# Kernel tuning notes

Measured on AMD Instinct MI355X. Metric: run time of the kernel, lower is better.

The kernel has to match this reference:

```python
import jax, jax.numpy as jnp
import numpy as np

B, T, D = 16, 512, 512
MEL_MAX = 4096


def setup_inputs() -> dict:
    key = jax.random.key(0)
    k0, k1, k2, k3 = jax.random.split(key, 4)
    x = jax.random.normal(k0, (B, T, D), dtype=jnp.float32)
    # integer frame durations per phoneme (the `target` used in training-mode LR)
    target = jax.random.randint(k1, (B, T), 0, 8, dtype=jnp.int32)
    scale = 1.0 / np.sqrt(D)
    W1 = jax.random.normal(k2, (D, D), dtype=jnp.float32) * scale
    b1 = jnp.zeros((D,), dtype=jnp.float32)
    W2 = jax.random.normal(k3, (D, 1), dtype=jnp.float32) * scale
    b2 = jnp.zeros((1,), dtype=jnp.float32)
    return {"x": x, "W1": W1, "b1": b1, "W2": W2, "b2": b2,
            "target": target, "mel_max_length": MEL_MAX}


def _length_regulate(x, durations, mel_max_length):
    """Vectorized repeat_interleave + pad.
    x: [B,T,D] float, durations: [B,T] int, output: [B,mel_max_length,D].
    Equivalent to per-batch torch expand+cat then pad, done via cumsum+searchsorted gather.
    """
    cs = jnp.cumsum(durations, axis=1)                    # [B,T] exclusive upper bounds
    pos = jnp.arange(mel_max_length)                      # [L]

    def expand_one(xb, csb):
        idx = jnp.searchsorted(csb, pos, side='right')    # [L] phoneme index per frame
        valid = pos < csb[-1]                             # frames beyond total -> pad
        idx = jnp.clip(idx, 0, xb.shape[0] - 1)
        return jnp.where(valid[:, None], xb[idx], jnp.zeros((), xb.dtype))

    return jax.vmap(expand_one)(x, cs)                    # [B,L,D]


def reference(x, W1, b1, W2, b2, target, mel_max_length):
    # DurationPredictor: Linear(512,512)+ReLU, Linear(512,1)+ReLU, squeeze -> [B,T]
    h = jax.nn.relu(jnp.einsum('btd,de->bte', x, W1) + b1)
    duration_predictor_output = jax.nn.relu(jnp.einsum('bte,eo->bto', h, W2) + b2)[..., 0]
    # Training-mode LR: expand x by integer `target` durations, pad to mel_max_length
    output = _length_regulate(x, target, mel_max_length)
    return output, duration_predictor_output
```

## Files before the change

### kernel.cpp

```cpp
#include <hip/hip_runtime.h>
#include <hip/hip_bf16.h>

#define BSZ 16
#define TT 512
#define DD 512
#define MM (BSZ * TT)
#define NPART 8
#define NMEGA 512

typedef __attribute__((ext_vector_type(8))) short bf16x8;
typedef __attribute__((ext_vector_type(8))) unsigned short ushort8;
typedef __attribute__((ext_vector_type(4))) float f32x4;

__global__ __launch_bounds__(256) void prep_kernel(const float* __restrict__ W1,
                                                   const int* __restrict__ target,
                                                   ushort* __restrict__ wth,
                                                   int* __restrict__ imap, int L) {
    int bid = blockIdx.x;
    if (bid < 256) {
        int t = bid * 256 + threadIdx.x;
        int n  = t & (DD - 1);
        int kq = t >> 9;
        ushort hh[4];
        #pragma unroll
        for (int i = 0; i < 4; ++i) {
            float f = W1[(size_t)(kq * 4 + i) * DD + n];
            __hip_bfloat16 bh = __float2bfloat16(f);
            hh[i] = *(ushort*)&bh;
        }
        ((ushort4*)wth)[(size_t)n * (DD / 4) + kq] = make_ushort4(hh[0], hh[1], hh[2], hh[3]);
    } else {
        int b = bid - 256;
        __shared__ int s[TT];
        int t = threadIdx.x;
        s[t]       = target[b * TT + t];
        s[t + 256] = target[b * TT + t + 256];
        __syncthreads();
        #pragma unroll
        for (int off = 1; off < TT; off <<= 1) {
            int v0 = (t >= off) ? s[t - off] : 0;
            int v1 = s[t + 256 - off];
            __syncthreads();
            s[t] += v0;
            s[t + 256] += v1;
            __syncthreads();
        }
        int total = s[TT - 1];
        int* imb = imap + (size_t)b * L;
        for (int ph = t; ph < TT; ph += 256) {
            int st = (ph == 0) ? 0 : s[ph - 1];
            int en = s[ph];
            for (int d = st; d < en; ++d) imb[d] = ph;
        }
        for (int l = total + t; l < L; l += 256) imb[l] = -1;
    }
}

#define BM 64
#define BN 128
#define BK 64
__global__ __launch_bounds__(256, 2) void mega_kernel(const ushort* __restrict__ wth,
                                                      const float* __restrict__ b1,
                                                      const float* __restrict__ W2,
                                                      const float* __restrict__ x,
                                                      const int* __restrict__ imap,
                                                      float* __restrict__ out,
                                                      float* __restrict__ partial,
                                                      int L) {
    __shared__ ushort ldsA[2][BM * 64];
    __shared__ ushort ldsB[2][BN * 64];
    const int bid = blockIdx.x;
    const int t = threadIdx.x;
    const int lane = t & 63, wave = t >> 6;
    const int row0 = (bid >> 2) * BM;
    const int col0 = (bid & 3) * BN;
    const int rq = t >> 3;
    const int ls = (t & 7) ^ (rq & 7);
    const int sco = ls * 8;
    const int ar = t >> 2;
    const int ac = (t & 3) * 16;

    const int b_lr    = bid >> 5;
    const int chunk0  = (bid & 31) * 128;
    const int lr_lane = t & 127;
    const int lr_half = t >> 7;
    const f32x4* x4g = (const f32x4*)(x + (size_t)b_lr * TT * DD);
    f32x4*       o4  = (f32x4*)(out + (size_t)b_lr * L * DD);
    const int*   imb = imap + (size_t)b_lr * L;

    auto stageB = [&](int buf, int kt) {
        const int k0 = kt * BK;
        #pragma unroll
        for (int q = 0; q < 4; ++q) {
            int row = q * 32 + rq;
            const ushort* gb = wth + (size_t)(col0 + row) * DD + k0 + sco;
            auto lb = (__attribute__((address_space(3))) unsigned int*)
                      ((char*)&ldsB[buf][0] + q * 4096 + wave * 1024);
            __builtin_amdgcn_global_load_lds(
                (const __attribute__((address_space(1))) unsigned int*)gb, lb, 16, 0, 0);
        }
    };
    auto stageA = [&](int buf, int kt) {
        const float* xa = x + (size_t)(row0 + ar) * DD + kt * BK + ac;
        float fl[16];
        *(f32x4*)&fl[0]  = ((const f32x4*)xa)[0];
        *(f32x4*)&fl[4]  = ((const f32x4*)xa)[1];
        *(f32x4*)&fl[8]  = ((const f32x4*)xa)[2];
        *(f32x4*)&fl[12] = ((const f32x4*)xa)[3];
        ushort us[16];
        #pragma unroll
        for (int j = 0; j < 16; ++j) {
            __hip_bfloat16 bh = __float2bfloat16(fl[j]);
            us[j] = *(ushort*)&bh;
        }
        int s0 = ((t & 3) * 2)     ^ (ar & 7);
        int s1 = ((t & 3) * 2 + 1) ^ (ar & 7);
        *(ushort8*)&ldsA[buf][ar * 64 + s0 * 8] = *(ushort8*)&us[0];
        *(ushort8*)&ldsA[buf][ar * 64 + s1 * 8] = *(ushort8*)&us[8];
    };

    const int wm = (wave >> 1) * 32;
    const int wn = (wave & 1) * 64;
    const int l15 = lane & 15, l4 = lane >> 4;
    f32x4 acc[2][4] = {};

    stageB(0, 0);
    stageA(0, 0);
    __syncthreads();
    int cur = 0;
    #pragma unroll 1
    for (int kt = 0; kt < DD / BK; ++kt) {
        if (kt + 1 < DD / BK) stageB(cur ^ 1, kt + 1);

        const int rb0 = chunk0 + kt * 16 + lr_half;
        int idxs[8];
        #pragma unroll
        for (int p = 0; p < 8; ++p) idxs[p] = imb[rb0 + p * 2];
        f32x4 gv[8];
        #pragma unroll
        for (int p = 0; p < 8; ++p)
            gv[p] = (idxs[p] >= 0) ? x4g[(size_t)idxs[p] * (DD / 4) + lr_lane]
                                   : (f32x4){0.f, 0.f, 0.f, 0.f};

        const ushort* At = &ldsA[cur][0];
        const ushort* Bt = &ldsB[cur][0];
        bf16x8 a[2][2], b[4][2];
        #pragma unroll
        for (int i = 0; i < 2; ++i) {
            int r = wm + i * 16 + l15;
            #pragma unroll
            for (int ks = 0; ks < 2; ++ks) {
                int sl = (ks * 4 + l4) ^ (r & 7);
                a[i][ks] = *(const bf16x8*)&At[r * 64 + sl * 8];
            }
        }
        #pragma unroll
        for (int j = 0; j < 4; ++j) {
            int r = wn + j * 16 + l15;
            #pragma unroll
            for (int ks = 0; ks < 2; ++ks) {
                int sl = (ks * 4 + l4) ^ (r & 7);
                b[j][ks] = *(const bf16x8*)&Bt[r * 64 + sl * 8];
            }
        }
        #pragma unroll
        for (int ks = 0; ks < 2; ++ks)
            #pragma unroll
            for (int i = 0; i < 2; ++i)
                #pragma unroll
                for (int j = 0; j < 4; ++j)
                    acc[i][j] = __builtin_amdgcn_mfma_f32_16x16x32_bf16(a[i][ks], b[j][ks], acc[i][j], 0, 0, 0);

        if (kt + 1 < DD / BK) stageA(cur ^ 1, kt + 1);

        #pragma unroll
        for (int p = 0; p < 8; ++p)
            __builtin_nontemporal_store(gv[p], &o4[(size_t)(rb0 + p * 2) * (DD / 4) + lr_lane]);

        __syncthreads();
        cur ^= 1;
    }

    const int pslice = (bid & 3) * 2 + (wn >> 6);
    #pragma unroll
    for (int i = 0; i < 2; ++i) {
        #pragma unroll
        for (int r = 0; r < 4; ++r) {
            float s = 0.f;
            #pragma unroll
            for (int j = 0; j < 4; ++j) {
                int cg = col0 + wn + j * 16 + l15;
                float h = acc[i][j][r] + b1[cg];
                h = fmaxf(h, 0.f);
                s += h * W2[cg];
            }
            s += __shfl_xor(s, 1);
            s += __shfl_xor(s, 2);
            s += __shfl_xor(s, 4);
            s += __shfl_xor(s, 8);
            if (l15 == 0) {
                int rg = row0 + wm + i * 16 + l4 * 4 + r;
                partial[(size_t)pslice * MM + rg] = s;
            }
        }
    }
}

__global__ __launch_bounds__(256) void dpo_kernel(const float* __restrict__ partial,
                                                  const float* __restrict__ b2,
                                                  float* __restrict__ dpo) {
    int m = blockIdx.x * 256 + threadIdx.x;
    float s = b2[0];
    #pragma unroll
    for (int nb = 0; nb < NPART; ++nb) s += partial[(size_t)nb * MM + m];
    dpo[m] = fmaxf(s, 0.f);
}

extern "C" void kernel_launch(void* const* d_in, const int* in_sizes, int n_in,
                              void* d_out, int out_size, void* d_ws, size_t ws_size,
                              hipStream_t stream) {
    const float* x      = (const float*)d_in[0];
    const float* W1     = (const float*)d_in[1];
    const float* b1     = (const float*)d_in[2];
    const float* W2     = (const float*)d_in[3];
    const float* b2     = (const float*)d_in[4];
    const int*   target = (const int*)d_in[5];
    int L = (out_size - BSZ * TT) / (BSZ * DD);

    float* out_lr  = (float*)d_out;
    float* out_dpo = (float*)d_out + (size_t)BSZ * L * DD;

    ushort* wth     = (ushort*)d_ws;
    float*  partial = (float*)(wth + (size_t)DD * DD);
    int*    imap    = (int*)(partial + (size_t)NPART * MM);

    prep_kernel<<<dim3(272), dim3(256), 0, stream>>>(W1, target, wth, imap, L);
    mega_kernel<<<dim3(NMEGA), dim3(256), 0, stream>>>(wth, b1, W2, x, imap,
                                                       out_lr, partial, L);
    dpo_kernel<<<dim3(MM / 256), dim3(256), 0, stream>>>(partial, b2, out_dpo);
}
```

Baseline: 43.04 us.

## Split mega kernel into independent GEMM waves and gather waves without LDS

Restructures the fused kernel so each block's first two waves each compute an independent 32x64 GEMM tile, reading A and B fragments straight from global memory with no LDS staging or barriers. The other two waves handle the length-regulation gather/copy on their own row chunks. The grid doubles to 1024 blocks and launch bounds allow 4 blocks per CU. This removes the __syncthreads coupling between the GEMM and the memory-bound copy, but drops LDS reuse, so operand reads come redundantly from global or L2.

```diff
diff --git a/kernel.cpp b/kernel.cpp
--- a/kernel.cpp
+++ b/kernel.cpp
@@ -6,10 +6,9 @@
 #define DD 512
 #define MM (BSZ * TT)
 #define NPART 8
-#define NMEGA 512
+#define NMEGA 1024
 
 typedef __attribute__((ext_vector_type(8))) short bf16x8;
-typedef __attribute__((ext_vector_type(8))) unsigned short ushort8;
 typedef __attribute__((ext_vector_type(4))) float f32x4;
 
 __global__ __launch_bounds__(256) void prep_kernel(const float* __restrict__ W1,
@@ -56,10 +55,7 @@
     }
 }
 
-#define BM 64
-#define BN 128
-#define BK 64
-__global__ __launch_bounds__(256, 2) void mega_kernel(const ushort* __restrict__ wth,
+__global__ __launch_bounds__(256, 4) void mega_kernel(const ushort* __restrict__ wth,
                                                       const float* __restrict__ b1,
                                                       const float* __restrict__ W2,
                                                       const float* __restrict__ x,
@@ -67,121 +63,71 @@
                                                       float* __restrict__ out,
                                                       float* __restrict__ partial,
                                                       int L) {
-    __shared__ ushort ldsA[2][BM * 64];
-    __shared__ ushort ldsB[2][BN * 64];
     const int bid = blockIdx.x;
     const int t = threadIdx.x;
     const int lane = t & 63, wave = t >> 6;
-    const int row0 = (bid >> 2) * BM;
-    const int col0 = (bid & 3) * BN;
-    const int rq = t >> 3;
-    const int ls = (t & 7) ^ (rq & 7);
-    const int sco = ls * 8;
-    const int ar = t >> 2;
-    const int ac = (t & 3) * 16;
 
-    const int b_lr    = bid >> 5;
-    const int chunk0  = (bid & 31) * 128;
-    const int lr_lane = t & 127;
-    const int lr_half = t >> 7;
-    const f32x4* x4g = (const f32x4*)(x + (size_t)b_lr * TT * DD);
-    f32x4*       o4  = (f32x4*)(out + (size_t)b_lr * L * DD);
-    const int*   imb = imap + (size_t)b_lr * L;
+    if (wave >= 2) {
+        const int h = bid * 2 + (wave - 2);
+        const int b_lr = h >> 7;
+        const int chunk = (h & 127) * 32;
+        const f32x4* x4g = (const f32x4*)(x + (size_t)b_lr * TT * DD);
+        f32x4*       o4  = (f32x4*)(out + (size_t)b_lr * L * DD);
+        const int*   imb = imap + (size_t)b_lr * L;
+        #pragma unroll 2
+        for (int r = 0; r < 32; ++r) {
+            int l = chunk + r;
+            int idx = imb[l];
+            f32x4 g0, g1;
+            if (idx >= 0) {
+                g0 = x4g[(size_t)idx * 128 + lane];
+                g1 = x4g[(size_t)idx * 128 + 64 + lane];
+            } else {
+                g0 = (f32x4){0.f, 0.f, 0.f, 0.f};
+                g1 = g0;
+            }
+            __builtin_nontemporal_store(g0, &o4[(size_t)l * 128 + lane]);
+            __builtin_nontemporal_store(g1, &o4[(size_t)l * 128 + 64 + lane]);
+        }
+        return;
+    }
 
-    auto stageB = [&](int buf, int kt) {
-        const int k0 = kt * BK;
-        #pragma unroll
-        for (int q = 0; q < 4; ++q) {
-            int row = q * 32 + rq;
-            const ushort* gb = wth + (size_t)(col0 + row) * DD + k0 + sco;
-            auto lb = (__attribute__((address_space(3))) unsigned int*)
-                      ((char*)&ldsB[buf][0] + q * 4096 + wave * 1024);
-            __builtin_amdgcn_global_load_lds(
-                (const __attribute__((address_space(1))) unsigned int*)gb, lb, 16, 0, 0);
-        }
-    };
-    auto stageA = [&](int buf, int kt) {
-        const float* xa = x + (size_t)(row0 + ar) * DD + kt * BK + ac;
-        float fl[16];
-        *(f32x4*)&fl[0]  = ((const f32x4*)xa)[0];
-        *(f32x4*)&fl[4]  = ((const f32x4*)xa)[1];
-        *(f32x4*)&fl[8]  = ((const f32x4*)xa)[2];
-        *(f32x4*)&fl[12] = ((const f32x4*)xa)[3];
-        ushort us[16];
-        #pragma unroll
-        for (int j = 0; j < 16; ++j) {
-            __hip_bfloat16 bh = __float2bfloat16(fl[j]);
-            us[j] = *(ushort*)&bh;
-        }
-        int s0 = ((t & 3) * 2)     ^ (ar & 7);
-        int s1 = ((t & 3) * 2 + 1) ^ (ar & 7);
-        *(ushort8*)&ldsA[buf][ar * 64 + s0 * 8] = *(ushort8*)&us[0];
-        *(ushort8*)&ldsA[buf][ar * 64 + s1 * 8] = *(ushort8*)&us[8];
-    };
-
-    const int wm = (wave >> 1) * 32;
-    const int wn = (wave & 1) * 64;
+    const int g = bid * 2 + wave;
+    const int rt = g >> 3, ct = g & 7;
+    const int row0 = rt * 32, col0 = ct * 64;
     const int l15 = lane & 15, l4 = lane >> 4;
     f32x4 acc[2][4] = {};
 
-    stageB(0, 0);
-    stageA(0, 0);
-    __syncthreads();
-    int cur = 0;
-    #pragma unroll 1
-    for (int kt = 0; kt < DD / BK; ++kt) {
-        if (kt + 1 < DD / BK) stageB(cur ^ 1, kt + 1);
-
-        const int rb0 = chunk0 + kt * 16 + lr_half;
-        int idxs[8];
-        #pragma unroll
-        for (int p = 0; p < 8; ++p) idxs[p] = imb[rb0 + p * 2];
-        f32x4 gv[8];
-        #pragma unroll
-        for (int p = 0; p < 8; ++p)
-            gv[p] = (idxs[p] >= 0) ? x4g[(size_t)idxs[p] * (DD / 4) + lr_lane]
-                                   : (f32x4){0.f, 0.f, 0.f, 0.f};
-
-        const ushort* At = &ldsA[cur][0];
-        const ushort* Bt = &ldsB[cur][0];
-        bf16x8 a[2][2], b[4][2];
+    #pragma unroll 2
+    for (int kt = 0; kt < DD / 32; ++kt) {
+        const int k0 = kt * 32;
+        bf16x8 af[2];
         #pragma unroll
         for (int i = 0; i < 2; ++i) {
-            int r = wm + i * 16 + l15;
+            const float* xa = x + (size_t)(row0 + i * 16 + l15) * DD + k0 + l4 * 8;
+            f32x4 f0 = ((const f32x4*)xa)[0];
+            f32x4 f1 = ((const f32x4*)xa)[1];
+            ushort us[8];
             #pragma unroll
-            for (int ks = 0; ks < 2; ++ks) {
-                int sl = (ks * 4 + l4) ^ (r & 7);
-                a[i][ks] = *(const bf16x8*)&At[r * 64 + sl * 8];
+            for (int e = 0; e < 4; ++e) {
+                __hip_bfloat16 h0 = __float2bfloat16(f0[e]);
+                __hip_bfloat16 h1 = __float2bfloat16(f1[e]);
+                us[e] = *(ushort*)&h0;
+                us[e + 4] = *(ushort*)&h1;
             }
+            af[i] = *(bf16x8*)us;
         }
+        bf16x8 bf[4];
         #pragma unroll
-        for (int j = 0; j < 4; ++j) {
-            int r = wn + j * 16 + l15;
+        for (int j = 0; j < 4; ++j)
+            bf[j] = *(const bf16x8*)&wth[(size_t)(col0 + j * 16 + l15) * DD + k0 + l4 * 8];
+        #pragma unroll
+        for (int i = 0; i < 2; ++i)
             #pragma unroll
-            for (int ks = 0; ks < 2; ++ks) {
-                int sl = (ks * 4 + l4) ^ (r & 7);
-                b[j][ks] = *(const bf16x8*)&Bt[r * 64 + sl * 8];
-            }
-        }
-        #pragma unroll
-        for (int ks = 0; ks < 2; ++ks)
-            #pragma unroll
-            for (int i = 0; i < 2; ++i)
-                #pragma unroll
-                for (int j = 0; j < 4; ++j)
-                    acc[i][j] = __builtin_amdgcn_mfma_f32_16x16x32_bf16(a[i][ks], b[j][ks], acc[i][j], 0, 0, 0);
-
-        if (kt + 1 < DD / BK) stageA(cur ^ 1, kt + 1);
-
-        #pragma unroll
-        for (int p = 0; p < 8; ++p)
-            __builtin_nontemporal_store(gv[p], &o4[(size_t)(rb0 + p * 2) * (DD / 4) + lr_lane]);
-
-        __syncthreads();
-        cur ^= 1;
+            for (int j = 0; j < 4; ++j)
+                acc[i][j] = __builtin_amdgcn_mfma_f32_16x16x32_bf16(af[i], bf[j], acc[i][j], 0, 0, 0);
     }
 
-    const int pslice = (bid & 3) * 2 + (wn >> 6);
     #pragma unroll
     for (int i = 0; i < 2; ++i) {
         #pragma unroll
@@ -189,7 +135,7 @@
             float s = 0.f;
             #pragma unroll
             for (int j = 0; j < 4; ++j) {
-                int cg = col0 + wn + j * 16 + l15;
+                int cg = col0 + j * 16 + l15;
                 float h = acc[i][j][r] + b1[cg];
                 h = fmaxf(h, 0.f);
                 s += h * W2[cg];
@@ -199,8 +145,8 @@
             s += __shfl_xor(s, 4);
             s += __shfl_xor(s, 8);
             if (l15 == 0) {
-                int rg = row0 + wm + i * 16 + l4 * 4 + r;
-                partial[(size_t)pslice * MM + rg] = s;
+                int rg = row0 + i * 16 + l4 * 4 + r;
+                partial[(size_t)ct * MM + rg] = s;
             }
         }
     }
```

After: 54.16 us. +25.9%, slower.
